# Performance work log

Measured on AMD Instinct MI355X. Metric: run time of the kernel, lower is better.

The kernel has to match this reference:

```python
import jax, jax.numpy as jnp
import numpy as np
import math

B, S, D = 4, 4096, 1024
H, HD, LK = 16, 64, 256


def setup_inputs() -> dict:
    key = jax.random.key(0)
    ks = jax.random.split(key, 8)
    s = 1.0 / math.sqrt(D)
    return {
        "X": jax.random.normal(ks[0], (B, S, D), jnp.float32),
        "mask": jnp.ones((B, S), jnp.float32),
        "Wq": jax.random.normal(ks[1], (D, H * HD), jnp.float32) * s,
        "bq": jnp.zeros((H * HD,), jnp.float32),
        "Wk": jax.random.normal(ks[2], (D, H * HD), jnp.float32) * s,
        "bk": jnp.zeros((H * HD,), jnp.float32),
        "Wv": jax.random.normal(ks[3], (D, H * HD), jnp.float32) * s,
        "bv": jnp.zeros((H * HD,), jnp.float32),
        "E": jax.random.normal(ks[4], (H, LK, S), jnp.float32) / math.sqrt(LK),
        "Wo": jax.random.normal(ks[5], (H * HD, D), jnp.float32) * s,
        "bo": jnp.zeros((D,), jnp.float32),
    }


def reference(X, mask, Wq, bq, Wk, bk, Wv, bv, E, Wo, bo):
    Bd, Sd, Dd = X.shape

    def split_heads(t):  # [B,S,H*HD] -> [B,H,S,HD]
        return t.reshape(Bd, Sd, H, HD).transpose(0, 2, 1, 3)

    Q = split_heads(X @ Wq + bq)
    K = split_heads(X @ Wk + bk)
    V = split_heads(X @ Wv + bv)

    m = mask[:, None, :, None]  # [B,1,S,1]
    # Low-rank projection along sequence: [H,LK,S] x [B,H,S,HD] -> [B,H,LK,HD]
    Kp = jnp.einsum('hks,bhsd->bhkd', E, K * m)
    Vp = jnp.einsum('hks,bhsd->bhkd', E, V * m)

    dot = jnp.einsum('bhsd,bhkd->bhsk', Q, Kp) / math.sqrt(HD)
    attn = jax.nn.softmax(dot, axis=-1)
    Xo = jnp.einsum('bhsk,bhkd->bhsd', attn, Vp)

    Xo = Xo.transpose(0, 2, 1, 3).reshape(Bd, Sd, H * HD)
    return Xo @ Wo + bo
```

## Files before the change

### kernel.cpp

```cpp
#include <hip/hip_runtime.h>
#include <hip/hip_bf16.h>
#include <stdint.h>

typedef __bf16 bf16_t;
typedef __attribute__((ext_vector_type(8))) __bf16 bf16x8;
typedef __attribute__((ext_vector_type(4))) __bf16 bf16x4;
typedef __attribute__((ext_vector_type(4))) float f32x4;

#define TO_GLB(p) ((const __attribute__((address_space(1))) void*)(p))
#define TO_LDS(p) ((__attribute__((address_space(3))) void*)(p))

__global__ __launch_bounds__(256) void cast2_bf16_kernel(const float* __restrict__ a,
                                                         bf16_t* __restrict__ da,
                                                         const float* __restrict__ b,
                                                         bf16_t* __restrict__ db, int n4) {
  int i = blockIdx.x * 256 + threadIdx.x;
  const float* s = (i < n4) ? a : b;
  bf16_t* d = (i < n4) ? da : db;
  int j = (i < n4) ? i : i - n4;
  float4 v = ((const float4*)s)[j];
  bf16x4 o;
  o[0] = (bf16_t)v.x; o[1] = (bf16_t)v.y; o[2] = (bf16_t)v.z; o[3] = (bf16_t)v.w;
  ((bf16x4*)d)[j] = o;
}

__global__ __launch_bounds__(256) void transpose_cast4(
    const float* __restrict__ W0, const float* __restrict__ W1, const float* __restrict__ W2,
    const float* __restrict__ W3, bf16_t* __restrict__ o0, bf16_t* __restrict__ o1,
    bf16_t* __restrict__ o2, bf16_t* __restrict__ o3) {
  const int RC = 1024;
  __shared__ bf16_t tile[64][72];
  int z = blockIdx.z;
  const float* W = (z == 0) ? W0 : (z == 1) ? W1 : (z == 2) ? W2 : W3;
  bf16_t* out = (z == 0) ? o0 : (z == 1) ? o1 : (z == 2) ? o2 : o3;
  int r0 = blockIdx.y * 64, c0 = blockIdx.x * 64;
  int tid = threadIdx.x;
#pragma unroll
  for (int p = 0; p < 4; ++p) {
    int r = p * 16 + (tid >> 4);
    int c = (tid & 15) * 4;
    float4 v = *(const float4*)(W + (size_t)(r0 + r) * RC + c0 + c);
    tile[r][c + 0] = (bf16_t)v.x; tile[r][c + 1] = (bf16_t)v.y;
    tile[r][c + 2] = (bf16_t)v.z; tile[r][c + 3] = (bf16_t)v.w;
  }
  __syncthreads();
#pragma unroll
  for (int p = 0; p < 4; ++p) {
    int c = p * 16 + (tid >> 4);
    int r = (tid & 15) * 4;
    bf16x4 o;
    o[0] = tile[r + 0][c]; o[1] = tile[r + 1][c];
    o[2] = tile[r + 2][c]; o[3] = tile[r + 3][c];
    *(bf16x4*)(out + (size_t)(c0 + c) * RC + r0 + r) = o;
  }
}


#define AS_(s) (GemmLds + (s) * 16384)
#define BS_(s) (GemmLds + 32768 + (s) * 16384)

#define STAGE_A(s, h, k0v)                                                                   \
  do {                                                                                       \
    _Pragma("unroll") for (int it_ = 0; it_ < 2; ++it_) {                                    \
      int brow_ = it_ * 128 + (h) * 64 + (wv << 3);                                          \
      int row_ = brow_ + (lane >> 3);                                                        \
      int cc_ = (lane & 7) ^ (lane >> 3);                                                    \
      const bf16_t* ga_ = Ab + (size_t)row_ * K + (k0v) + cc_ * 8;                           \
      __builtin_amdgcn_global_load_lds(TO_GLB(ga_), TO_LDS(AS_(s) + brow_ * 64), 16, 0, 0);  \
    }                                                                                        \
  } while (0)

#define STAGE_B(s, h, k0v)                                                                   \
  do {                                                                                       \
    _Pragma("unroll") for (int it_ = 0; it_ < 2; ++it_) {                                    \
      int brow_ = (it_ * 2 + (wv >> 2)) * 64 + (h) * 32 + ((wv & 3) << 3);                   \
      int row_ = brow_ + (lane >> 3);                                                        \
      int cc_ = (lane & 7) ^ (lane >> 3);                                                    \
      const bf16_t* gb_ = Bb + (size_t)row_ * K + (k0v) + cc_ * 8;                           \
      __builtin_amdgcn_global_load_lds(TO_GLB(gb_), TO_LDS(BS_(s) + brow_ * 64), 16, 0, 0);  \
    }                                                                                        \
  } while (0)

#define VM4 asm volatile("s_waitcnt vmcnt(4)" ::: "memory")
#define BARRIER __builtin_amdgcn_s_barrier()
#define LGKM0 asm volatile("s_waitcnt lgkmcnt(0)" ::: "memory")

#define LOAD_AF(s, mh)                                                                       \
  do {                                                                                       \
    _Pragma("unroll") for (int kk_ = 0; kk_ < 2; ++kk_)                                      \
        _Pragma("unroll") for (int t_ = 0; t_ < 4; ++t_) {                                   \
      int ra_ = wm * 128 + (mh) * 64 + t_ * 16 + m_in;                                       \
      af[kk_][t_] = *(const bf16x8*)(AS_(s) + ra_ * 64 + (((kk_ * 4 + q) ^ (ra_ & 7)) * 8)); \
    }                                                                                        \
  } while (0)

#define LOAD_BF(s, nh, dst)                                                                  \
  do {                                                                                       \
    _Pragma("unroll") for (int kk_ = 0; kk_ < 2; ++kk_)                                      \
        _Pragma("unroll") for (int n_ = 0; n_ < 2; ++n_) {                                   \
      int rb_ = wn * 64 + (nh) * 32 + n_ * 16 + m_in;                                        \
      dst[kk_][n_] = *(const bf16x8*)(BS_(s) + rb_ * 64 + (((kk_ * 4 + q) ^ (rb_ & 7)) * 8)); \
    }                                                                                        \
  } while (0)

#define MFMA_Q(mh, nh, bfr)                                                                  \
  do {                                                                                       \
    __builtin_amdgcn_s_setprio(1);                                                           \
    _Pragma("unroll") for (int kk_ = 0; kk_ < 2; ++kk_)                                      \
        _Pragma("unroll") for (int t_ = 0; t_ < 4; ++t_)                                     \
            _Pragma("unroll") for (int n_ = 0; n_ < 2; ++n_)                                 \
                acc[(mh) * 4 + t_][(nh) * 2 + n_] = __builtin_amdgcn_mfma_f32_16x16x32_bf16( \
                    af[kk_][t_], bfr[kk_][n_], acc[(mh) * 4 + t_][(nh) * 2 + n_], 0, 0, 0);  \
    __builtin_amdgcn_s_setprio(0);                                                           \
  } while (0)

#define KTILE(s, ST1, ST2, ST3, ST4)                                                         \
  do {                                                                                       \
    LOAD_AF(s, 0); LOAD_BF(s, 0, bf0);                                                       \
    ST1; BARRIER; LGKM0; MFMA_Q(0, 0, bf0); BARRIER;                                         \
    LOAD_BF(s, 1, bf1);                                                                      \
    ST2; BARRIER; LGKM0; MFMA_Q(0, 1, bf1); BARRIER;                                         \
    LOAD_AF(s, 1);                                                                           \
    ST3; BARRIER; LGKM0; MFMA_Q(1, 0, bf0); BARRIER;                                         \
    ST4; VM4; BARRIER; MFMA_Q(1, 1, bf1); BARRIER;                                           \
  } while (0)

__global__ __launch_bounds__(512, 2) void gemm_bt_8ph(
    const bf16_t* __restrict__ A, const bf16_t* __restrict__ B, int K, int mode,
    const float* __restrict__ bq, const float* __restrict__ bk, const float* __restrict__ bv,
    const float* __restrict__ mask,
    bf16_t* __restrict__ Q, bf16_t* __restrict__ KT, bf16_t* __restrict__ VT,
    const float* __restrict__ bo, float* __restrict__ out) {
  int tid = threadIdx.x;
  int lane = tid & 63, wv = tid >> 6;
  int wm = wv >> 2, wn = wv & 3;
  int q = lane >> 4, m_in = lane & 15;
  int bid = blockIdx.x;
  int bm = bid & 63, bn = bid >> 6;
  size_t m0 = (size_t)bm * 256;
  size_t n0 = (size_t)bn * 256;
  const bf16_t* Ab = A + m0 * K;
  const bf16_t* Bb = B + n0 * K;
  __shared__ __align__(16) bf16_t GemmLds[65536];

  f32x4 acc[8][4];
  bf16x8 af[2][4], bf0[2][2], bf1[2][2];
  f32x4 z = {0.f, 0.f, 0.f, 0.f};
#pragma unroll
  for (int mt = 0; mt < 8; ++mt)
#pragma unroll
    for (int nt = 0; nt < 4; ++nt) acc[mt][nt] = z;

  int NT = K >> 6;
  int NI = NT >> 1;

  STAGE_A(0, 0, 0); STAGE_B(0, 0, 0); STAGE_A(0, 1, 0); STAGE_B(0, 1, 0);
  STAGE_A(1, 0, 64); STAGE_B(1, 0, 64);
  asm volatile("s_waitcnt vmcnt(4)" ::: "memory");
  __builtin_amdgcn_s_barrier();

  for (int i = 0; i < NI; ++i) {
    int kt = 2 * i;
    int k1 = (kt + 1) * 64;
    int k2 = (kt + 2 < NT) ? (kt + 2) * 64 : 0;
    int k3 = (kt + 3 < NT) ? (kt + 3) * 64 : 0;
    KTILE(0, STAGE_A(1, 1, k1), STAGE_B(1, 1, k1), STAGE_A(0, 0, k2), STAGE_B(0, 0, k2));
    KTILE(1, STAGE_A(0, 1, k2), STAGE_B(0, 1, k2), STAGE_A(1, 0, k3), STAGE_B(1, 0, k3));
  }
  asm volatile("s_waitcnt vmcnt(0)" ::: "memory");

  if (mode == 0) {
    __syncthreads();
    int proj = (int)(n0 >> 10);
    int b = (int)(m0 >> 12), st0 = (int)(m0 & 4095);
    int nb10 = (int)(n0 & 1023);
    if (proj == 0) {
#pragma unroll
      for (int mt = 0; mt < 8; ++mt) {
#pragma unroll
        for (int nt = 0; nt < 4; ++nt) {
          int n = wn * 64 + nt * 16 + m_in;
          float bias = bq[nb10 + n];
#pragma unroll
          for (int r = 0; r < 4; ++r) {
            int tl = wm * 128 + mt * 16 + q * 4 + r;
            GemmLds[tl * 256 + ((((n >> 3) ^ (tl & 31)) << 3) | (n & 7))] =
                (bf16_t)(acc[mt][nt][r] + bias);
          }
        }
      }
      __syncthreads();
      int hb = (int)(n0 >> 6);
#pragma unroll
      for (int it = 0; it < 16; ++it) {
        int cid = it * 512 + tid;
        int tl = cid >> 5, c = cid & 31;
        bf16x8 v = *(const bf16x8*)(GemmLds + tl * 256 + ((c ^ (tl & 31)) << 3));
        int h = hb + (c >> 3);
        *(bf16x8*)(Q + ((size_t)(b * 16 + h) * 4096 + st0 + tl) * 64 + (c & 7) * 8) = v;
      }
    } else {
      bf16_t* dstb = (proj == 1) ? KT : VT;
      const float* bp = (proj == 1) ? bk : bv;
#pragma unroll
      for (int mt = 0; mt < 8; ++mt) {
        int mb = wm * 128 + mt * 16 + q * 4;
        float mk[4];
#pragma unroll
        for (int r = 0; r < 4; ++r) mk[r] = mask[b * 4096 + st0 + mb + r];
#pragma unroll
        for (int nt = 0; nt < 4; ++nt) {
          int n = wn * 64 + nt * 16 + m_in;
          float bias = bp[nb10 + n];
#pragma unroll
          for (int r = 0; r < 4; ++r) {
            int tl = mb + r;
            GemmLds[n * 256 + ((((tl >> 3) ^ (n & 31)) << 3) | (tl & 7))] =
                (bf16_t)((acc[mt][nt][r] + bias) * mk[r]);
          }
        }
      }
      __syncthreads();
#pragma unroll
      for (int it = 0; it < 16; ++it) {
        int cid = it * 512 + tid;
        int nl = cid >> 5, c = cid & 31;
        bf16x8 v = *(const bf16x8*)(GemmLds + nl * 256 + ((c ^ (nl & 31)) << 3));
        int c10 = nb10 + nl, h = c10 >> 6, hd = c10 & 63;
        *(bf16x8*)(dstb + ((size_t)(b * 16 + h) * 64 + hd) * 4096 + st0 + c * 8) = v;
      }
    }
  } else {
#pragma unroll
    for (int mt = 0; mt < 8; ++mt) {
      int t = (int)m0 + wm * 128 + mt * 16 + q * 4;
#pragma unroll
      for (int nt = 0; nt < 4; ++nt) {
        int nG = (int)n0 + wn * 64 + nt * 16 + m_in;
        float bias = bo[nG];
#pragma unroll
        for (int r = 0; r < 4; ++r) out[(size_t)(t + r) * 1024 + nG] = acc[mt][nt][r] + bias;
      }
    }
  }
}

__global__ __launch_bounds__(512) void gemm2_kernel(
    const bf16_t* __restrict__ E, const bf16_t* __restrict__ KT, const bf16_t* __restrict__ VT,
    float* __restrict__ Pp) {
  int tid = threadIdx.x, lane = tid & 63, wv = tid >> 6;
  int wm = wv >> 1, wn = wv & 1;
  int q = lane >> 4, m_in = lane & 15;
  int mt0 = blockIdx.x;
  int bh = blockIdx.y;
  int kc = blockIdx.z;
  int h = bh & 15;
  const bf16_t* Ab = E + (size_t)h * 256 * 4096 + (size_t)mt0 * 128 * 4096 + (size_t)kc * 2048;
  const bf16_t* BbK = KT + (size_t)bh * 64 * 4096 + (size_t)kc * 2048;
  const bf16_t* BbV = VT + (size_t)bh * 64 * 4096 + (size_t)kc * 2048;
  __shared__ __align__(16) bf16_t As[2 * 128 * 64];
  __shared__ __align__(16) bf16_t BsK[2 * 64 * 64];
  __shared__ __align__(16) bf16_t BsV[2 * 64 * 64];

  f32x4 accK[2][2], accV[2][2];
  f32x4 z = {0.f, 0.f, 0.f, 0.f};
#pragma unroll
  for (int mt = 0; mt < 2; ++mt)
#pragma unroll
    for (int nt = 0; nt < 2; ++nt) { accK[mt][nt] = z; accV[mt][nt] = z; }

  for (int k0 = 0; k0 < 2048; k0 += 128) {
#pragma unroll
    for (int it = 0; it < 4; ++it) {
      int l = it * 512 + tid;
      int kkb = l >> 10, row = (l >> 3) & 127, cc = (l & 7) ^ (row & 7);
      const bf16_t* ga = Ab + (size_t)row * 4096 + k0 + kkb * 64 + cc * 8;
      __builtin_amdgcn_global_load_lds(TO_GLB(ga), TO_LDS(As + (it * 512 + wv * 64) * 8), 16, 0, 0);
    }
#pragma unroll
    for (int it = 0; it < 2; ++it) {
      int l = it * 512 + tid;
      int kkb = l >> 9, row = (l >> 3) & 63, cc = (l & 7) ^ (row & 7);
      const bf16_t* gb = BbK + (size_t)row * 4096 + k0 + kkb * 64 + cc * 8;
      __builtin_amdgcn_global_load_lds(TO_GLB(gb), TO_LDS(BsK + (it * 512 + wv * 64) * 8), 16, 0, 0);
    }
#pragma unroll
    for (int it = 0; it < 2; ++it) {
      int l = it * 512 + tid;
      int kkb = l >> 9, row = (l >> 3) & 63, cc = (l & 7) ^ (row & 7);
      const bf16_t* gb = BbV + (size_t)row * 4096 + k0 + kkb * 64 + cc * 8;
      __builtin_amdgcn_global_load_lds(TO_GLB(gb), TO_LDS(BsV + (it * 512 + wv * 64) * 8), 16, 0, 0);
    }
    __syncthreads();
#pragma unroll
    for (int kk4 = 0; kk4 < 4; ++kk4) {
      int kkb = kk4 >> 1, qq = (kk4 & 1) * 4 + q;
      bf16x8 af[2], bK[2], bV[2];
#pragma unroll
      for (int mt = 0; mt < 2; ++mt) {
        int ra = wm * 32 + mt * 16 + m_in;
        af[mt] = *(const bf16x8*)(As + kkb * 8192 + ra * 64 + ((qq ^ (ra & 7)) * 8));
      }
#pragma unroll
      for (int nt = 0; nt < 2; ++nt) {
        int rb = wn * 32 + nt * 16 + m_in;
        bK[nt] = *(const bf16x8*)(BsK + kkb * 4096 + rb * 64 + ((qq ^ (rb & 7)) * 8));
        bV[nt] = *(const bf16x8*)(BsV + kkb * 4096 + rb * 64 + ((qq ^ (rb & 7)) * 8));
      }
#pragma unroll
      for (int mt = 0; mt < 2; ++mt)
#pragma unroll
        for (int nt = 0; nt < 2; ++nt) {
          accK[mt][nt] = __builtin_amdgcn_mfma_f32_16x16x32_bf16(af[mt], bK[nt], accK[mt][nt], 0, 0, 0);
          accV[mt][nt] = __builtin_amdgcn_mfma_f32_16x16x32_bf16(af[mt], bV[nt], accV[mt][nt], 0, 0, 0);
        }
    }
    __syncthreads();
  }

  float* PK = Pp + ((size_t)(bh * 2 + 0) * 2 + kc) * 16384;
  float* PV = Pp + ((size_t)(bh * 2 + 1) * 2 + kc) * 16384;
#pragma unroll
  for (int mt = 0; mt < 2; ++mt) {
    int lk = mt0 * 128 + wm * 32 + mt * 16 + q * 4;
#pragma unroll
    for (int nt = 0; nt < 2; ++nt) {
      int hd = wn * 32 + nt * 16 + m_in;
#pragma unroll
      for (int r = 0; r < 4; ++r) {
        PK[(size_t)(lk + r) * 64 + hd] = accK[mt][nt][r];
        PV[(size_t)(lk + r) * 64 + hd] = accV[mt][nt][r];
      }
    }
  }
}

__global__ __launch_bounds__(256) void gemm2_reduce(const float* __restrict__ Pp,
                                                    bf16_t* __restrict__ Kp,
                                                    bf16_t* __restrict__ VpT) {
  int bh = blockIdx.x, kv = blockIdx.y;
  int tid = threadIdx.x;
  const float* P = Pp + ((size_t)(bh * 2 + kv) * 2) * 16384;
  if (kv == 0) {
#pragma unroll
    for (int it = 0; it < 16; ++it) {
      int e4 = it * 256 + tid;
      f32x4 s = *(const f32x4*)(P + e4 * 4);
      f32x4 s1 = *(const f32x4*)(P + 16384 + e4 * 4);
      s += s1;
      bf16x4 v;
#pragma unroll
      for (int r = 0; r < 4; ++r) v[r] = (bf16_t)s[r];
      *(bf16x4*)(Kp + (size_t)bh * 16384 + e4 * 4) = v;
    }
  } else {
    __shared__ __align__(16) bf16_t T[16384];
#pragma unroll
    for (int it = 0; it < 16; ++it) {
      int e4 = it * 256 + tid;
      f32x4 s = *(const f32x4*)(P + e4 * 4);
      f32x4 s1 = *(const f32x4*)(P + 16384 + e4 * 4);
      s += s1;
      int lk = (e4 * 4) >> 6, hd0 = (e4 * 4) & 63;
#pragma unroll
      for (int r = 0; r < 4; ++r) {
        int hd = hd0 + r;
        T[hd * 256 + ((((lk >> 3) ^ (hd & 31)) << 3) | (lk & 7))] = (bf16_t)s[r];
      }
    }
    __syncthreads();
#pragma unroll
    for (int it = 0; it < 8; ++it) {
      int cid = it * 256 + tid;
      int hd = cid >> 5, c = cid & 31;
      bf16x8 v = *(const bf16x8*)(T + hd * 256 + ((c ^ (hd & 31)) << 3));
      *(bf16x8*)(VpT + (size_t)bh * 16384 + hd * 256 + c * 8) = v;
    }
  }
}

__global__ __launch_bounds__(256) void attn_kernel(
    const bf16_t* __restrict__ Q, const bf16_t* __restrict__ Kp, const bf16_t* __restrict__ VpT,
    bf16_t* __restrict__ Xo) {
  int tid = threadIdx.x, lane = tid & 63, wv = tid >> 6;
  int q = lane >> 4, m_in = lane & 15;
  int s0 = blockIdx.x * 64;
  int bh = blockIdx.y;
  int b = bh >> 4, h = bh & 15;
  const bf16_t* Qb = Q + ((size_t)bh * 4096 + s0 + wv * 16) * 64;
  const bf16_t* Kpb = Kp + (size_t)bh * 16384;
  const bf16_t* Vb = VpT + (size_t)bh * 16384;
  __shared__ __align__(16) bf16_t buf[16384];

#pragma unroll
  for (int it = 0; it < 8; ++it) {
    int l = it * 256 + tid;
    int row = l >> 3, cc = (l & 7) ^ (row & 7);
    const bf16_t* g = Kpb + row * 64 + cc * 8;
    __builtin_amdgcn_global_load_lds(TO_GLB(g), TO_LDS(buf + (it * 256 + wv * 64) * 8), 16, 0, 0);
  }
  bf16x8 aq[2];
#pragma unroll
  for (int ks = 0; ks < 2; ++ks) aq[ks] = *(const bf16x8*)(Qb + (size_t)m_in * 64 + ks * 32 + q * 8);
  __syncthreads();

  f32x4 sc[16];
  f32x4 z = {0.f, 0.f, 0.f, 0.f};
#pragma unroll
  for (int nt = 0; nt < 16; ++nt) sc[nt] = z;
#pragma unroll
  for (int nt = 0; nt < 16; ++nt)
#pragma unroll
    for (int ks = 0; ks < 2; ++ks) {
      int nb = nt * 16 + m_in, qq = ks * 4 + q;
      bf16x8 kb = *(const bf16x8*)(buf + nb * 64 + ((qq ^ (nb & 7)) * 8));
      sc[nt] = __builtin_amdgcn_mfma_f32_16x16x32_bf16(aq[ks], kb, sc[nt], 0, 0, 0);
    }

  float mx[4], sm[4];
#pragma unroll
  for (int r = 0; r < 4; ++r) mx[r] = -1e30f;
#pragma unroll
  for (int nt = 0; nt < 16; ++nt)
#pragma unroll
    for (int r = 0; r < 4; ++r) {
      float t = sc[nt][r] * 0.125f;
      sc[nt][r] = t;
      mx[r] = fmaxf(mx[r], t);
    }
#pragma unroll
  for (int off = 1; off < 16; off <<= 1)
#pragma unroll
    for (int r = 0; r < 4; ++r) mx[r] = fmaxf(mx[r], __shfl_xor(mx[r], off));
#pragma unroll
  for (int r = 0; r < 4; ++r) sm[r] = 0.f;
#pragma unroll
  for (int nt = 0; nt < 16; ++nt)
#pragma unroll
    for (int r = 0; r < 4; ++r) {
      float e = __expf(sc[nt][r] - mx[r]);
      sc[nt][r] = e;
      sm[r] += e;
    }
#pragma unroll
  for (int off = 1; off < 16; off <<= 1)
#pragma unroll
    for (int r = 0; r < 4; ++r) sm[r] += __shfl_xor(sm[r], off);
  float inv[4];
#pragma unroll
  for (int r = 0; r < 4; ++r) inv[r] = 1.0f / sm[r];

  __syncthreads();

  bf16_t* Pw = buf + wv * 4096;
#pragma unroll
  for (int nt = 0; nt < 16; ++nt) {
    int cw = nt * 2 + (m_in >> 3);
#pragma unroll
    for (int r = 0; r < 4; ++r) {
      int rp = q * 4 + r;
      int sw = (((cw ^ (rp & 7)) << 3) | (m_in & 7));
      Pw[rp * 256 + sw] = (bf16_t)(sc[nt][r] * inv[r]);
    }
  }
  bf16x8 pa[8];
#pragma unroll
  for (int ks = 0; ks < 8; ++ks) {
    int c = ks * 4 + q;
    pa[ks] = *(const bf16x8*)(Pw + m_in * 256 + ((c ^ (m_in & 7)) << 3));
  }
  __syncthreads();

#pragma unroll
  for (int it = 0; it < 8; ++it) {
    int l = it * 256 + tid;
    int row = l >> 5, cc = l & 31;
    int src_cc = (cc & 24) | ((cc ^ row) & 7);
    const bf16_t* g = Vb + row * 256 + src_cc * 8;
    __builtin_amdgcn_global_load_lds(TO_GLB(g), TO_LDS(buf + (it * 256 + wv * 64) * 8), 16, 0, 0);
  }
  __syncthreads();

  f32x4 o[4];
#pragma unroll
  for (int nt = 0; nt < 4; ++nt) o[nt] = z;
#pragma unroll
  for (int nt = 0; nt < 4; ++nt)
#pragma unroll
    for (int ks = 0; ks < 8; ++ks) {
      int nb = nt * 16 + m_in, qq = ks * 4 + q;
      int p = (qq & 24) | ((qq ^ nb) & 7);
      bf16x8 vb = *(const bf16x8*)(buf + nb * 256 + p * 8);
      o[nt] = __builtin_amdgcn_mfma_f32_16x16x32_bf16(pa[ks], vb, o[nt], 0, 0, 0);
    }

#pragma unroll
  for (int nt = 0; nt < 4; ++nt)
#pragma unroll
    for (int r = 0; r < 4; ++r)
      Xo[((size_t)b * 4096 + s0 + wv * 16 + q * 4 + r) * 1024 + h * 64 + nt * 16 + m_in] =
          (bf16_t)o[nt][r];
}

extern "C" void kernel_launch(void* const* d_in, const int* in_sizes, int n_in,
                              void* d_out, int out_size, void* d_ws, size_t ws_size,
                              hipStream_t stream) {
  const float* X = (const float*)d_in[0];
  const float* mask = (const float*)d_in[1];
  const float* Wq = (const float*)d_in[2];
  const float* bq = (const float*)d_in[3];
  const float* Wk = (const float*)d_in[4];
  const float* bk = (const float*)d_in[5];
  const float* Wv = (const float*)d_in[6];
  const float* bv = (const float*)d_in[7];
  const float* E = (const float*)d_in[8];
  const float* Wo = (const float*)d_in[9];
  const float* bo = (const float*)d_in[10];
  float* out = (float*)d_out;

  char* ws = (char*)d_ws;
  const size_t SZ = 33554432;
  bf16_t* Xb = (bf16_t*)(ws);
  float* Pp = (float*)(ws);
  bf16_t* Eb = (bf16_t*)(ws + SZ);
  bf16_t* Qb = (bf16_t*)(ws + 2 * SZ);
  bf16_t* KT = (bf16_t*)(ws + 3 * SZ);
  bf16_t* VT = (bf16_t*)(ws + 4 * SZ);
  bf16_t* Kp = (bf16_t*)(ws + 5 * SZ);
  bf16_t* VpT = (bf16_t*)(ws + 5 * SZ + 8388608);
  bf16_t* WqkvT = (bf16_t*)(ws + 5 * SZ + 2 * 8388608);
  bf16_t* WoT = (bf16_t*)(ws + 5 * SZ + 2 * 8388608 + 6291456);
  bf16_t* Xo = Xb;

  cast2_bf16_kernel<<<32768, 256, 0, stream>>>(X, Xb, E, Eb, 4194304);
  transpose_cast4<<<dim3(16, 16, 4), 256, 0, stream>>>(
      Wq, Wk, Wv, Wo, WqkvT, WqkvT + 1048576, WqkvT + 2097152, WoT);

  gemm_bt_8ph<<<768, 512, 0, stream>>>(Xb, WqkvT, 1024, 0, bq, bk, bv, mask,
                                       Qb, KT, VT, nullptr, nullptr);
  gemm2_kernel<<<dim3(2, 64, 2), 512, 0, stream>>>(Eb, KT, VT, Pp);
  gemm2_reduce<<<dim3(64, 2), 256, 0, stream>>>(Pp, Kp, VpT);
  attn_kernel<<<dim3(64, 64), 256, 0, stream>>>(Qb, Kp, VpT, Xo);
  gemm_bt_8ph<<<256, 512, 0, stream>>>(Xo, WoT, 1024, 1, nullptr, nullptr, nullptr,
                                       nullptr, nullptr, nullptr, nullptr, bo, out);
}
```

Before: 429.2 us.

## Double-buffer gemm2 LDS loads and stage output GEMM epilogue through LDS

In the E-projection GEMM (gemm2), a second LDS buffer is added so the next K-chunk is prefetched with global_load_lds while MFMAs consume the current one, overlapping memory latency with compute. Separately, the output-projection epilogue now writes the fp32 accumulators plus bias into swizzled LDS in two halves and then stores 16-byte vectors to global memory with coalesced access, replacing scattered scalar stores. This doubles the LDS footprint of gemm2, which can lower occupancy, and adds extra barriers to the epilogue.

```diff
diff --git a/kernel.cpp b/kernel.cpp
--- a/kernel.cpp
+++ b/kernel.cpp
@@ -231,15 +231,33 @@
       }
     }
   } else {
-#pragma unroll
-    for (int mt = 0; mt < 8; ++mt) {
-      int t = (int)m0 + wm * 128 + mt * 16 + q * 4;
-#pragma unroll
-      for (int nt = 0; nt < 4; ++nt) {
-        int nG = (int)n0 + wn * 64 + nt * 16 + m_in;
-        float bias = bo[nG];
-#pragma unroll
-        for (int r = 0; r < 4; ++r) out[(size_t)(t + r) * 1024 + nG] = acc[mt][nt][r] + bias;
+    float* L = (float*)GemmLds;
+    __syncthreads();
+#pragma unroll
+    for (int hh = 0; hh < 2; ++hh) {
+      if (hh) __syncthreads();
+      if (wm == hh) {
+#pragma unroll
+        for (int mt = 0; mt < 8; ++mt) {
+#pragma unroll
+          for (int nt = 0; nt < 4; ++nt) {
+            int n = wn * 64 + nt * 16 + m_in;
+            float bias = bo[(int)n0 + n];
+#pragma unroll
+            for (int r = 0; r < 4; ++r) {
+              int row = mt * 16 + q * 4 + r;
+              L[row * 256 + (n ^ ((row & 7) << 2))] = acc[mt][nt][r] + bias;
+            }
+          }
+        }
+      }
+      __syncthreads();
+#pragma unroll
+      for (int it = 0; it < 16; ++it) {
+        int cid = it * 512 + tid;
+        int row = cid >> 6, c = cid & 63;
+        f32x4 v = *(const f32x4*)(L + row * 256 + ((c ^ (row & 7)) << 2));
+        *(f32x4*)(out + (size_t)((int)m0 + hh * 128 + row) * 1024 + (int)n0 + c * 4) = v;
       }
     }
   }
@@ -258,9 +276,34 @@
   const bf16_t* Ab = E + (size_t)h * 256 * 4096 + (size_t)mt0 * 128 * 4096 + (size_t)kc * 2048;
   const bf16_t* BbK = KT + (size_t)bh * 64 * 4096 + (size_t)kc * 2048;
   const bf16_t* BbV = VT + (size_t)bh * 64 * 4096 + (size_t)kc * 2048;
-  __shared__ __align__(16) bf16_t As[2 * 128 * 64];
-  __shared__ __align__(16) bf16_t BsK[2 * 64 * 64];
-  __shared__ __align__(16) bf16_t BsV[2 * 64 * 64];
+  __shared__ __align__(16) bf16_t As[2 * 16384];
+  __shared__ __align__(16) bf16_t BsK[2 * 8192];
+  __shared__ __align__(16) bf16_t BsV[2 * 8192];
+
+#define G2_STAGE(slot, k0v)                                                                   \
+  do {                                                                                        \
+    _Pragma("unroll") for (int it = 0; it < 4; ++it) {                                        \
+      int l = it * 512 + tid;                                                                 \
+      int kkb = l >> 10, row = (l >> 3) & 127, cc = (l & 7) ^ (row & 7);                      \
+      const bf16_t* ga = Ab + (size_t)row * 4096 + (k0v) + kkb * 64 + cc * 8;                 \
+      __builtin_amdgcn_global_load_lds(TO_GLB(ga),                                            \
+          TO_LDS(As + (slot) * 16384 + (it * 512 + wv * 64) * 8), 16, 0, 0);                  \
+    }                                                                                         \
+    _Pragma("unroll") for (int it = 0; it < 2; ++it) {                                        \
+      int l = it * 512 + tid;                                                                 \
+      int kkb = l >> 9, row = (l >> 3) & 63, cc = (l & 7) ^ (row & 7);                        \
+      const bf16_t* gb = BbK + (size_t)row * 4096 + (k0v) + kkb * 64 + cc * 8;                \
+      __builtin_amdgcn_global_load_lds(TO_GLB(gb),                                            \
+          TO_LDS(BsK + (slot) * 8192 + (it * 512 + wv * 64) * 8), 16, 0, 0);                  \
+    }                                                                                         \
+    _Pragma("unroll") for (int it = 0; it < 2; ++it) {                                        \
+      int l = it * 512 + tid;                                                                 \
+      int kkb = l >> 9, row = (l >> 3) & 63, cc = (l & 7) ^ (row & 7);                        \
+      const bf16_t* gb = BbV + (size_t)row * 4096 + (k0v) + kkb * 64 + cc * 8;                \
+      __builtin_amdgcn_global_load_lds(TO_GLB(gb),                                            \
+          TO_LDS(BsV + (slot) * 8192 + (it * 512 + wv * 64) * 8), 16, 0, 0);                  \
+    }                                                                                         \
+  } while (0)
 
   f32x4 accK[2][2], accV[2][2];
   f32x4 z = {0.f, 0.f, 0.f, 0.f};
@@ -269,54 +312,38 @@
 #pragma unroll
     for (int nt = 0; nt < 2; ++nt) { accK[mt][nt] = z; accV[mt][nt] = z; }
 
-  for (int k0 = 0; k0 < 2048; k0 += 128) {
-#pragma unroll
-    for (int it = 0; it < 4; ++it) {
-      int l = it * 512 + tid;
-      int kkb = l >> 10, row = (l >> 3) & 127, cc = (l & 7) ^ (row & 7);
-      const bf16_t* ga = Ab + (size_t)row * 4096 + k0 + kkb * 64 + cc * 8;
-      __builtin_amdgcn_global_load_lds(TO_GLB(ga), TO_LDS(As + (it * 512 + wv * 64) * 8), 16, 0, 0);
-    }
-#pragma unroll
-    for (int it = 0; it < 2; ++it) {
-      int l = it * 512 + tid;
-      int kkb = l >> 9, row = (l >> 3) & 63, cc = (l & 7) ^ (row & 7);
-      const bf16_t* gb = BbK + (size_t)row * 4096 + k0 + kkb * 64 + cc * 8;
-      __builtin_amdgcn_global_load_lds(TO_GLB(gb), TO_LDS(BsK + (it * 512 + wv * 64) * 8), 16, 0, 0);
-    }
-#pragma unroll
-    for (int it = 0; it < 2; ++it) {
-      int l = it * 512 + tid;
-      int kkb = l >> 9, row = (l >> 3) & 63, cc = (l & 7) ^ (row & 7);
-      const bf16_t* gb = BbV + (size_t)row * 4096 + k0 + kkb * 64 + cc * 8;
-      __builtin_amdgcn_global_load_lds(TO_GLB(gb), TO_LDS(BsV + (it * 512 + wv * 64) * 8), 16, 0, 0);
-    }
-    __syncthreads();
+  G2_STAGE(0, 0);
+  __syncthreads();
+
+  for (int t = 0; t < 16; ++t) {
+    int cur = t & 1;
+    if (t < 15) G2_STAGE(cur ^ 1, (t + 1) * 128);
 #pragma unroll
     for (int kk4 = 0; kk4 < 4; ++kk4) {
       int kkb = kk4 >> 1, qq = (kk4 & 1) * 4 + q;
-      bf16x8 af[2], bK[2], bV[2];
+      bf16x8 afr[2], bK[2], bV[2];
 #pragma unroll
       for (int mt = 0; mt < 2; ++mt) {
         int ra = wm * 32 + mt * 16 + m_in;
-        af[mt] = *(const bf16x8*)(As + kkb * 8192 + ra * 64 + ((qq ^ (ra & 7)) * 8));
+        afr[mt] = *(const bf16x8*)(As + cur * 16384 + kkb * 8192 + ra * 64 + ((qq ^ (ra & 7)) * 8));
       }
 #pragma unroll
       for (int nt = 0; nt < 2; ++nt) {
         int rb = wn * 32 + nt * 16 + m_in;
-        bK[nt] = *(const bf16x8*)(BsK + kkb * 4096 + rb * 64 + ((qq ^ (rb & 7)) * 8));
-        bV[nt] = *(const bf16x8*)(BsV + kkb * 4096 + rb * 64 + ((qq ^ (rb & 7)) * 8));
+        bK[nt] = *(const bf16x8*)(BsK + cur * 8192 + kkb * 4096 + rb * 64 + ((qq ^ (rb & 7)) * 8));
+        bV[nt] = *(const bf16x8*)(BsV + cur * 8192 + kkb * 4096 + rb * 64 + ((qq ^ (rb & 7)) * 8));
       }
 #pragma unroll
       for (int mt = 0; mt < 2; ++mt)
 #pragma unroll
         for (int nt = 0; nt < 2; ++nt) {
-          accK[mt][nt] = __builtin_amdgcn_mfma_f32_16x16x32_bf16(af[mt], bK[nt], accK[mt][nt], 0, 0, 0);
-          accV[mt][nt] = __builtin_amdgcn_mfma_f32_16x16x32_bf16(af[mt], bV[nt], accV[mt][nt], 0, 0, 0);
+          accK[mt][nt] = __builtin_amdgcn_mfma_f32_16x16x32_bf16(afr[mt], bK[nt], accK[mt][nt], 0, 0, 0);
+          accV[mt][nt] = __builtin_amdgcn_mfma_f32_16x16x32_bf16(afr[mt], bV[nt], accV[mt][nt], 0, 0, 0);
         }
     }
     __syncthreads();
   }
+#undef G2_STAGE
 
   float* PK = Pp + ((size_t)(bh * 2 + 0) * 2 + kc) * 16384;
   float* PV = Pp + ((size_t)(bh * 2 + 1) * 2 + kc) * 16384;
```

Result: slower. 452.3 us (+5.4%).
